# Performance work log

Hardware: AMD Instinct MI355X
Metric: run time of the kernel (lower is better)

The kernel has to match this reference:

```python
import jax, jax.numpy as jnp
import numpy as np

N, D, E = 40000, 128, 640000
SLOPE = 0.01  # torch LeakyReLU default negative_slope

def leaky(x):
    return jnp.where(x >= 0, x, SLOPE * x)

def setup_inputs() -> dict:
    key = jax.random.key(0)
    ks = jax.random.split(key, 12)
    s = lambda fan_in: 1.0 / np.sqrt(fan_in)
    inp = {
        "x": jax.random.normal(ks[0], (N, D), jnp.float32),
        "pos": jax.random.normal(ks[1], (N, 3), jnp.float32),
        "edge_index": jax.random.randint(ks[2], (2, E), 0, N, jnp.int64),
        # mlp_h: Linear(D,D) -> LeakyReLU -> Linear(D,3) -> Tanh
        "Wh1": jax.random.uniform(ks[3], (D, D), jnp.float32, -s(D), s(D)),
        "bh1": jnp.zeros((D,), jnp.float32),
        "Wh2": jax.random.uniform(ks[4], (D, 3), jnp.float32, -s(D), s(D)),
        "bh2": jnp.zeros((3,), jnp.float32),
        # mlp_f: Linear(D+3, D) -> LeakyReLU
        "Wf1": jax.random.uniform(ks[5], (D + 3, D), jnp.float32, -s(D + 3), s(D + 3)),
        "bf1": jnp.zeros((D,), jnp.float32),
        # mlp_g: Linear(D,D) -> LeakyReLU -> Linear(D,D)
        "Wg1": jax.random.uniform(ks[6], (D, D), jnp.float32, -s(D), s(D)),
        "bg1": jnp.zeros((D,), jnp.float32),
        "Wg2": jax.random.uniform(ks[7], (D, D), jnp.float32, -s(D), s(D)),
        "bg2": jnp.zeros((D,), jnp.float32),
    }
    return inp

def reference(x, pos, edge_index, Wh1, bh1, Wh2, bh2, Wf1, bf1, Wg1, bg1, Wg2, bg2):
    src = edge_index[0]  # j (source / neighbor)
    dst = edge_index[1]  # i (target / center)
    n = x.shape[0]
    # mlp_h per node: predicted position offset delta_i
    delta = jnp.tanh(leaky(x @ Wh1 + bh1) @ Wh2 + bh2)  # [N, 3]
    # per-edge message: mlp_f(cat(pos_j - pos_i + delta_i, x_j))
    rel = pos[src] - pos[dst] + delta[dst]               # [E, 3]
    e = jnp.concatenate([rel, x[src]], axis=-1)          # [E, D+3]
    msg = leaky(e @ Wf1 + bf1)                           # [E, D]
    # sum aggregation to target nodes
    aggr = jax.ops.segment_sum(msg, dst, num_segments=n) # [N, D]
    # node update with residual
    out = x + (leaky(aggr @ Wg1 + bg1) @ Wg2 + bg2)      # [N, D]
    return out
```

## Files before the change

### kernel.cpp

```cpp
#include <hip/hip_runtime.h>

#define NN 40000
#define DD 128
#define EE 640000
#define SLOPE 0.01f
#define CAP 64

typedef __attribute__((ext_vector_type(8))) short  short8;
typedef __attribute__((ext_vector_type(8))) unsigned short ushort8;
typedef __attribute__((ext_vector_type(4))) float  floatx4;

__device__ __forceinline__ float leaky1(float v) { return v >= 0.f ? v : v * SLOPE; }

__device__ __forceinline__ unsigned short f2bf(float f) {
    unsigned int u = __float_as_uint(f);
    u += 0x7fffu + ((u >> 16) & 1u);
    return (unsigned short)(u >> 16);
}

__global__ __launch_bounds__(256) void k_init(
    const float* __restrict__ Wh1, const float* __restrict__ Wf1,
    const float* __restrict__ Wg1, const float* __restrict__ Wg2,
    int* __restrict__ cnt, unsigned short* __restrict__ pk)
{
    const int gid = blockIdx.x * 256 + threadIdx.x;
    if (gid < NN) cnt[gid] = 0;

    if (gid < 8192) {
        const int mat = gid >> 11;
        const int rem = gid & 2047;
        const int ct  = rem >> 8;
        const int kc  = (rem >> 6) & 3;
        const int l   = rem & 63;
        const float* W = (mat == 0) ? Wh1 : (mat == 1) ? (Wf1 + 3 * DD)
                       : (mat == 2) ? Wg1 : Wg2;
        const int n  = ct * 16 + (l & 15);
        const int k0 = kc * 32 + (l >> 4) * 8;
        ushort8 v;
        #pragma unroll
        for (int j = 0; j < 8; ++j) v[j] = f2bf(W[(size_t)(k0 + j) * DD + n]);
        *(ushort8*)(pk + (size_t)gid * 8) = v;
    }
}

__global__ __launch_bounds__(512) void k_pre_scatter(
    const float* __restrict__ x,
    const unsigned short* __restrict__ pk,
    const float* __restrict__ pos, const float* __restrict__ Wf1,
    const float* __restrict__ bh1, const float* __restrict__ Wh2,
    const float* __restrict__ bh2, const float* __restrict__ bf1,
    const int* __restrict__ ei,
    unsigned short* __restrict__ ub, float* __restrict__ delta,
    int* __restrict__ cnt, unsigned short* __restrict__ esrc)
{
    __shared__ unsigned short xt[64 * 136];
    __shared__ unsigned short ul[64 * 136];
    const int bid = blockIdx.x;
    const int t   = threadIdx.x;

    if (bid >= 625) {
        const int g   = bid & 7;
        const int lb  = (bid - 625) >> 3;
        const int dlo = g * 5000;
        const int dhi = dlo + 5000;

        for (int e = (lb * 512 + t) * 2; e < EE; e += 262144) {
            const int2 dp = *(const int2*)(ei + EE + e);
            const int2 sp = *(const int2*)(ei + e);
            if (dp.x >= dlo && dp.x < dhi) {
                const int p = atomicAdd(&cnt[dp.x], 1);
                if (p < CAP) esrc[(size_t)dp.x * CAP + p] = (unsigned short)sp.x;
            }
            if (dp.y >= dlo && dp.y < dhi) {
                const int p = atomicAdd(&cnt[dp.y], 1);
                if (p < CAP) esrc[(size_t)dp.y * CAP + p] = (unsigned short)sp.y;
            }
        }
        return;
    }

    const int w  = t >> 6, l = t & 63;
    const int lm = l & 15, q = l >> 4;
    const int rowb = bid * 64;

    {
        const int row = t >> 3;
        const int c0  = (t & 7) * 16;
        const float* xp = x + (size_t)(rowb + row) * DD + c0;
        #pragma unroll
        for (int p = 0; p < 2; ++p) {
            const float4 v0 = *(const float4*)(xp + p * 8);
            const float4 v1 = *(const float4*)(xp + p * 8 + 4);
            ushort8 o;
            o[0] = f2bf(v0.x); o[1] = f2bf(v0.y); o[2] = f2bf(v0.z); o[3] = f2bf(v0.w);
            o[4] = f2bf(v1.x); o[5] = f2bf(v1.y); o[6] = f2bf(v1.z); o[7] = f2bf(v1.w);
            *(ushort8*)(xt + row * 136 + c0 + p * 8) = o;
        }
    }
    __syncthreads();

    const bool upath = w < 4;
    const int wl   = upath ? w : w - 4;
    const int row0 = wl * 16;
    const unsigned short* pkm = upath ? (pk + 16384) : pk;

    floatx4 acc[8];
    #pragma unroll
    for (int ct = 0; ct < 8; ++ct) acc[ct] = 0.f;

    #pragma unroll
    for (int kc = 0; kc < 4; ++kc) {
        const short8 a = *(const short8*)(xt + (row0 + lm) * 136 + kc * 32 + q * 8);
        #pragma unroll
        for (int ct = 0; ct < 8; ++ct) {
            const short8 b = *(const short8*)(pkm + (size_t)((ct * 4 + kc) * 64 + l) * 8);
            acc[ct] = __builtin_amdgcn_mfma_f32_16x16x32_bf16(a, b, acc[ct], 0, 0, 0);
        }
    }

    if (upath) {
        float px[4][3];
        #pragma unroll
        for (int r = 0; r < 4; ++r) {
            const int rr = rowb + row0 + q * 4 + r;
            px[r][0] = pos[rr * 3 + 0];
            px[r][1] = pos[rr * 3 + 1];
            px[r][2] = pos[rr * 3 + 2];
        }
        #pragma unroll
        for (int ct = 0; ct < 8; ++ct) {
            const int col = ct * 16 + lm;
            const float bfv = bf1[col];
            const float w0 = Wf1[0 * DD + col];
            const float w1 = Wf1[1 * DD + col];
            const float w2 = Wf1[2 * DD + col];
            #pragma unroll
            for (int r = 0; r < 4; ++r) {
                const float uv = acc[ct][r] + bfv
                               + px[r][0] * w0 + px[r][1] * w1 + px[r][2] * w2;
                ul[(row0 + q * 4 + r) * 136 + col] = f2bf(uv);
            }
        }
    } else {
        float p[4][3] = {};
        #pragma unroll
        for (int ct = 0; ct < 8; ++ct) {
            const int col = ct * 16 + lm;
            const float b1 = bh1[col];
            const float wh20 = Wh2[col * 3 + 0];
            const float wh21 = Wh2[col * 3 + 1];
            const float wh22 = Wh2[col * 3 + 2];
            #pragma unroll
            for (int r = 0; r < 4; ++r) {
                const float hv = leaky1(acc[ct][r] + b1);
                p[r][0] += hv * wh20;
                p[r][1] += hv * wh21;
                p[r][2] += hv * wh22;
            }
        }
        #pragma unroll
        for (int m = 1; m < 16; m <<= 1) {
            #pragma unroll
            for (int r = 0; r < 4; ++r) {
                #pragma unroll
                for (int k = 0; k < 3; ++k)
                    p[r][k] += __shfl_xor(p[r][k], m);
            }
        }
        if (lm < 12) {
            const int r = lm / 3, k = lm - 3 * (lm / 3);
            delta[(size_t)(rowb + row0 + q * 4 + r) * 3 + k] = tanhf(p[r][k] + bh2[k]);
        }
    }
    __syncthreads();

    #pragma unroll
    for (int k = 0; k < 2; ++k) {
        const int idx = t + k * 512;
        const int row = idx >> 4;
        const int c8  = (idx & 15) * 8;
        *(ushort8*)(ub + (size_t)(rowb + row) * DD + c8) =
            *(const ushort8*)(ul + row * 136 + c8);
    }
}

__global__ __launch_bounds__(256) void k_gather(
    const int* __restrict__ cnt, const unsigned short* __restrict__ esrc,
    const float* __restrict__ pos, const float* __restrict__ delta,
    const float* __restrict__ Wf1, const unsigned short* __restrict__ ub,
    unsigned short* __restrict__ aggrb)
{
    const int t    = threadIdx.x;
    const int lane = t & 63;
    const int n    = blockIdx.x * 4 + (t >> 6);
    const int grp  = lane >> 4;
    const int li   = lane & 15;
    const int c    = li * 8;

    const float q0 = delta[n * 3 + 0] - pos[n * 3 + 0];
    const float q1 = delta[n * 3 + 1] - pos[n * 3 + 1];
    const float q2 = delta[n * 3 + 2] - pos[n * 3 + 2];

    float v[8];
    #pragma unroll
    for (int h = 0; h < 2; ++h) {
        const float4 w0 = *(const float4*)(Wf1 + 0 * DD + c + h * 4);
        const float4 w1 = *(const float4*)(Wf1 + 1 * DD + c + h * 4);
        const float4 w2 = *(const float4*)(Wf1 + 2 * DD + c + h * 4);
        v[h * 4 + 0] = q0 * w0.x + q1 * w1.x + q2 * w2.x;
        v[h * 4 + 1] = q0 * w0.y + q1 * w1.y + q2 * w2.y;
        v[h * 4 + 2] = q0 * w0.z + q1 * w1.z + q2 * w2.z;
        v[h * 4 + 3] = q0 * w0.w + q1 * w1.w + q2 * w2.w;
    }

    const int s_all = (int)esrc[(size_t)n * CAP + lane];
    const int d = min(cnt[n], CAP);

    float a[8] = {0.f, 0.f, 0.f, 0.f, 0.f, 0.f, 0.f, 0.f};

    for (int j = 0; j < d; j += 16) {
        uint4 u[4];
        bool vld[4];
        #pragma unroll
        for (int k = 0; k < 4; ++k) {
            const int e = j + 4 * k + grp;
            vld[k] = e < d;
            int src = __shfl(s_all, e & 63);
            src = vld[k] ? src : 0;
            u[k] = *(const uint4*)(ub + (size_t)src * DD + c);
        }
        #pragma unroll
        for (int k = 0; k < 4; ++k) {
            if (vld[k]) {
                const unsigned int uu0 = u[k].x, uu1 = u[k].y, uu2 = u[k].z, uu3 = u[k].w;
                const float e0 = __uint_as_float(uu0 << 16)         + v[0];
                const float e1 = __uint_as_float(uu0 & 0xffff0000u) + v[1];
                const float e2 = __uint_as_float(uu1 << 16)         + v[2];
                const float e3 = __uint_as_float(uu1 & 0xffff0000u) + v[3];
                const float e4 = __uint_as_float(uu2 << 16)         + v[4];
                const float e5 = __uint_as_float(uu2 & 0xffff0000u) + v[5];
                const float e6 = __uint_as_float(uu3 << 16)         + v[6];
                const float e7 = __uint_as_float(uu3 & 0xffff0000u) + v[7];
                a[0] += fmaxf(e0, e0 * SLOPE);
                a[1] += fmaxf(e1, e1 * SLOPE);
                a[2] += fmaxf(e2, e2 * SLOPE);
                a[3] += fmaxf(e3, e3 * SLOPE);
                a[4] += fmaxf(e4, e4 * SLOPE);
                a[5] += fmaxf(e5, e5 * SLOPE);
                a[6] += fmaxf(e6, e6 * SLOPE);
                a[7] += fmaxf(e7, e7 * SLOPE);
            }
        }
    }

    #pragma unroll
    for (int i = 0; i < 8; ++i) {
        a[i] += __shfl_xor(a[i], 16);
        a[i] += __shfl_xor(a[i], 32);
    }

    if (grp == 0) {
        uint4 st;
        st.x = ((unsigned int)f2bf(a[1]) << 16) | (unsigned int)f2bf(a[0]);
        st.y = ((unsigned int)f2bf(a[3]) << 16) | (unsigned int)f2bf(a[2]);
        st.z = ((unsigned int)f2bf(a[5]) << 16) | (unsigned int)f2bf(a[4]);
        st.w = ((unsigned int)f2bf(a[7]) << 16) | (unsigned int)f2bf(a[6]);
        *(uint4*)(aggrb + (size_t)n * DD + c) = st;
    }
}

__global__ __launch_bounds__(256) void k_node_out(
    const unsigned short* __restrict__ aggrb, const unsigned short* __restrict__ pk,
    const float* __restrict__ x,
    const float* __restrict__ bg1, const float* __restrict__ bg2,
    float* __restrict__ out)
{
    __shared__ unsigned short gl[64 * 136];
    __shared__ float          ol[64 * 132];
    const int t  = threadIdx.x;
    const int w  = t >> 6, l = t & 63;
    const int lm = l & 15, q = l >> 4;
    const int rowb = blockIdx.x * 64;
    const int row0 = rowb + w * 16;

    const unsigned short* pkg1 = pk + 32768;
    const unsigned short* pkg2 = pk + 49152;

    floatx4 gacc[8];
    #pragma unroll
    for (int ct = 0; ct < 8; ++ct) gacc[ct] = 0.f;

    #pragma unroll
    for (int kc = 0; kc < 4; ++kc) {
        const short8 a = *(const short8*)(aggrb + (size_t)(row0 + lm) * DD + kc * 32 + q * 8);
        #pragma unroll
        for (int ct = 0; ct < 8; ++ct) {
            const short8 b = *(const short8*)(pkg1 + (size_t)((ct * 4 + kc) * 64 + l) * 8);
            gacc[ct] = __builtin_amdgcn_mfma_f32_16x16x32_bf16(a, b, gacc[ct], 0, 0, 0);
        }
    }

    #pragma unroll
    for (int ct = 0; ct < 8; ++ct) {
        const int col = ct * 16 + lm;
        const float b1 = bg1[col];
        #pragma unroll
        for (int r = 0; r < 4; ++r)
            gl[(w * 16 + q * 4 + r) * 136 + col] = f2bf(leaky1(gacc[ct][r] + b1));
    }
    __syncthreads();

    floatx4 oacc[8];
    #pragma unroll
    for (int ct = 0; ct < 8; ++ct) oacc[ct] = 0.f;

    #pragma unroll
    for (int kc = 0; kc < 4; ++kc) {
        const short8 a = *(const short8*)(gl + (size_t)(w * 16 + lm) * 136 + kc * 32 + q * 8);
        #pragma unroll
        for (int ct = 0; ct < 8; ++ct) {
            const short8 b = *(const short8*)(pkg2 + (size_t)((ct * 4 + kc) * 64 + l) * 8);
            oacc[ct] = __builtin_amdgcn_mfma_f32_16x16x32_bf16(a, b, oacc[ct], 0, 0, 0);
        }
    }

    __syncthreads();
    #pragma unroll
    for (int ct = 0; ct < 8; ++ct) {
        const int col = ct * 16 + lm;
        #pragma unroll
        for (int r = 0; r < 4; ++r)
            ol[(w * 16 + q * 4 + r) * 132 + col] = oacc[ct][r];
    }
    __syncthreads();

    #pragma unroll
    for (int k = 0; k < 8; ++k) {
        const int idx = t + k * 256;
        const int row = idx >> 5;
        const int c4  = (idx & 31) * 4;
        const float4 ov = *(const float4*)(ol + row * 132 + c4);
        const float4 bv = *(const float4*)(bg2 + c4);
        const size_t o  = (size_t)(rowb + row) * DD + c4;
        const float4 xv = *(const float4*)(x + o);
        float4 rv;
        rv.x = xv.x + ov.x + bv.x;
        rv.y = xv.y + ov.y + bv.y;
        rv.z = xv.z + ov.z + bv.z;
        rv.w = xv.w + ov.w + bv.w;
        *(float4*)(out + o) = rv;
    }
}

extern "C" void kernel_launch(void* const* d_in, const int* in_sizes, int n_in,
                              void* d_out, int out_size, void* d_ws, size_t ws_size,
                              hipStream_t stream)
{
    const float* x   = (const float*)d_in[0];
    const float* pos = (const float*)d_in[1];
    const int*   ei  = (const int*)d_in[2];
    const float* Wh1 = (const float*)d_in[3];
    const float* bh1 = (const float*)d_in[4];
    const float* Wh2 = (const float*)d_in[5];
    const float* bh2 = (const float*)d_in[6];
    const float* Wf1 = (const float*)d_in[7];
    const float* bf1 = (const float*)d_in[8];
    const float* Wg1 = (const float*)d_in[9];
    const float* bg1 = (const float*)d_in[10];
    const float* Wg2 = (const float*)d_in[11];
    const float* bg2 = (const float*)d_in[12];
    float* out = (float*)d_out;

    unsigned short* ub    = (unsigned short*)d_ws;
    unsigned short* aggrb = ub + (size_t)NN * DD;
    unsigned short* pk    = aggrb + (size_t)NN * DD;
    float* delta = (float*)(pk + 65536);
    int*   cnt   = (int*)(delta + (size_t)NN * 3);
    unsigned short* esrc = (unsigned short*)(cnt + NN);

    k_init<<<160, 256, 0, stream>>>(Wh1, Wf1, Wg1, Wg2, cnt, pk);
    k_pre_scatter<<<2673, 512, 0, stream>>>(x, pk, pos, Wf1, bh1, Wh2, bh2, bf1,
                                            ei, ub, delta, cnt, esrc);
    k_gather<<<NN / 4, 256, 0, stream>>>(cnt, esrc, pos, delta, Wf1, ub, aggrb);
    k_node_out<<<NN / 64, 256, 0, stream>>>(aggrb, pk, x, bg1, bg2, out);
}
```

Baseline: 167.7 us.

## Fuse edge gather-aggregation into node output kernel, keeping aggregates in LDS

Merges the per-node gather/aggregation kernel with the node-update MLP kernel. Each wave now aggregates 16 nodes one after another and writes the bf16 sums into shared memory, reusing the output staging buffer. The MFMA GEMMs then read those sums from LDS instead of a global buffer. This removes one launch and the global round trip for the aggregate, but shrinks the grid from 10000 blocks to 625. That leaves far fewer waves in flight to hide latency in the memory-bound gather.

```diff
diff --git a/kernel.cpp b/kernel.cpp
--- a/kernel.cpp
+++ b/kernel.cpp
@@ -184,107 +184,110 @@
     }
 }
 
-__global__ __launch_bounds__(256) void k_gather(
+__global__ __launch_bounds__(256) void k_gather_out(
     const int* __restrict__ cnt, const unsigned short* __restrict__ esrc,
     const float* __restrict__ pos, const float* __restrict__ delta,
     const float* __restrict__ Wf1, const unsigned short* __restrict__ ub,
-    unsigned short* __restrict__ aggrb)
-{
-    const int t    = threadIdx.x;
-    const int lane = t & 63;
-    const int n    = blockIdx.x * 4 + (t >> 6);
-    const int grp  = lane >> 4;
-    const int li   = lane & 15;
-    const int c    = li * 8;
-
-    const float q0 = delta[n * 3 + 0] - pos[n * 3 + 0];
-    const float q1 = delta[n * 3 + 1] - pos[n * 3 + 1];
-    const float q2 = delta[n * 3 + 2] - pos[n * 3 + 2];
-
-    float v[8];
-    #pragma unroll
-    for (int h = 0; h < 2; ++h) {
-        const float4 w0 = *(const float4*)(Wf1 + 0 * DD + c + h * 4);
-        const float4 w1 = *(const float4*)(Wf1 + 1 * DD + c + h * 4);
-        const float4 w2 = *(const float4*)(Wf1 + 2 * DD + c + h * 4);
-        v[h * 4 + 0] = q0 * w0.x + q1 * w1.x + q2 * w2.x;
-        v[h * 4 + 1] = q0 * w0.y + q1 * w1.y + q2 * w2.y;
-        v[h * 4 + 2] = q0 * w0.z + q1 * w1.z + q2 * w2.z;
-        v[h * 4 + 3] = q0 * w0.w + q1 * w1.w + q2 * w2.w;
-    }
-
-    const int s_all = (int)esrc[(size_t)n * CAP + lane];
-    const int d = min(cnt[n], CAP);
-
-    float a[8] = {0.f, 0.f, 0.f, 0.f, 0.f, 0.f, 0.f, 0.f};
-
-    for (int j = 0; j < d; j += 16) {
-        uint4 u[4];
-        bool vld[4];
-        #pragma unroll
-        for (int k = 0; k < 4; ++k) {
-            const int e = j + 4 * k + grp;
-            vld[k] = e < d;
-            int src = __shfl(s_all, e & 63);
-            src = vld[k] ? src : 0;
-            u[k] = *(const uint4*)(ub + (size_t)src * DD + c);
-        }
-        #pragma unroll
-        for (int k = 0; k < 4; ++k) {
-            if (vld[k]) {
-                const unsigned int uu0 = u[k].x, uu1 = u[k].y, uu2 = u[k].z, uu3 = u[k].w;
-                const float e0 = __uint_as_float(uu0 << 16)         + v[0];
-                const float e1 = __uint_as_float(uu0 & 0xffff0000u) + v[1];
-                const float e2 = __uint_as_float(uu1 << 16)         + v[2];
-                const float e3 = __uint_as_float(uu1 & 0xffff0000u) + v[3];
-                const float e4 = __uint_as_float(uu2 << 16)         + v[4];
-                const float e5 = __uint_as_float(uu2 & 0xffff0000u) + v[5];
-                const float e6 = __uint_as_float(uu3 << 16)         + v[6];
-                const float e7 = __uint_as_float(uu3 & 0xffff0000u) + v[7];
-                a[0] += fmaxf(e0, e0 * SLOPE);
-                a[1] += fmaxf(e1, e1 * SLOPE);
-                a[2] += fmaxf(e2, e2 * SLOPE);
-                a[3] += fmaxf(e3, e3 * SLOPE);
-                a[4] += fmaxf(e4, e4 * SLOPE);
-                a[5] += fmaxf(e5, e5 * SLOPE);
-                a[6] += fmaxf(e6, e6 * SLOPE);
-                a[7] += fmaxf(e7, e7 * SLOPE);
-            }
-        }
-    }
-
-    #pragma unroll
-    for (int i = 0; i < 8; ++i) {
-        a[i] += __shfl_xor(a[i], 16);
-        a[i] += __shfl_xor(a[i], 32);
-    }
-
-    if (grp == 0) {
-        uint4 st;
-        st.x = ((unsigned int)f2bf(a[1]) << 16) | (unsigned int)f2bf(a[0]);
-        st.y = ((unsigned int)f2bf(a[3]) << 16) | (unsigned int)f2bf(a[2]);
-        st.z = ((unsigned int)f2bf(a[5]) << 16) | (unsigned int)f2bf(a[4]);
-        st.w = ((unsigned int)f2bf(a[7]) << 16) | (unsigned int)f2bf(a[6]);
-        *(uint4*)(aggrb + (size_t)n * DD + c) = st;
-    }
-}
-
-__global__ __launch_bounds__(256) void k_node_out(
-    const unsigned short* __restrict__ aggrb, const unsigned short* __restrict__ pk,
+    const unsigned short* __restrict__ pk,
     const float* __restrict__ x,
     const float* __restrict__ bg1, const float* __restrict__ bg2,
     float* __restrict__ out)
 {
     __shared__ unsigned short gl[64 * 136];
     __shared__ float          ol[64 * 132];
-    const int t  = threadIdx.x;
-    const int w  = t >> 6, l = t & 63;
-    const int lm = l & 15, q = l >> 4;
+    unsigned short* agg = (unsigned short*)ol;
+
+    const int t    = threadIdx.x;
+    const int w    = t >> 6, l = t & 63;
+    const int lane = l;
+    const int grp  = lane >> 4;
+    const int li   = lane & 15;
+    const int c    = li * 8;
+    const int lm   = l & 15, q = l >> 4;
     const int rowb = blockIdx.x * 64;
-    const int row0 = rowb + w * 16;
+
+    float wf[3][8];
+    #pragma unroll
+    for (int r = 0; r < 3; ++r) {
+        const float4 va = *(const float4*)(Wf1 + r * DD + c);
+        const float4 vb = *(const float4*)(Wf1 + r * DD + c + 4);
+        wf[r][0] = va.x; wf[r][1] = va.y; wf[r][2] = va.z; wf[r][3] = va.w;
+        wf[r][4] = vb.x; wf[r][5] = vb.y; wf[r][6] = vb.z; wf[r][7] = vb.w;
+    }
+
+    for (int nn = 0; nn < 16; ++nn) {
+        const int lrow = w * 16 + nn;
+        const int n    = rowb + lrow;
+
+        const float q0 = delta[n * 3 + 0] - pos[n * 3 + 0];
+        const float q1 = delta[n * 3 + 1] - pos[n * 3 + 1];
+        const float q2 = delta[n * 3 + 2] - pos[n * 3 + 2];
+
+        float v[8];
+        #pragma unroll
+        for (int i = 0; i < 8; ++i)
+            v[i] = q0 * wf[0][i] + q1 * wf[1][i] + q2 * wf[2][i];
+
+        const int s_all = (int)esrc[(size_t)n * CAP + lane];
+        const int d = min(cnt[n], CAP);
+
+        float a[8] = {0.f, 0.f, 0.f, 0.f, 0.f, 0.f, 0.f, 0.f};
+
+        for (int j = 0; j < d; j += 16) {
+            uint4 u[4];
+            bool vld[4];
+            #pragma unroll
+            for (int k = 0; k < 4; ++k) {
+                const int e = j + 4 * k + grp;
+                vld[k] = e < d;
+                int src = __shfl(s_all, e & 63);
+                src = vld[k] ? src : 0;
+                u[k] = *(const uint4*)(ub + (size_t)src * DD + c);
+            }
+            #pragma unroll
+            for (int k = 0; k < 4; ++k) {
+                if (vld[k]) {
+                    const unsigned int uu0 = u[k].x, uu1 = u[k].y, uu2 = u[k].z, uu3 = u[k].w;
+                    const float e0 = __uint_as_float(uu0 << 16)         + v[0];
+                    const float e1 = __uint_as_float(uu0 & 0xffff0000u) + v[1];
+                    const float e2 = __uint_as_float(uu1 << 16)         + v[2];
+                    const float e3 = __uint_as_float(uu1 & 0xffff0000u) + v[3];
+                    const float e4 = __uint_as_float(uu2 << 16)         + v[4];
+                    const float e5 = __uint_as_float(uu2 & 0xffff0000u) + v[5];
+                    const float e6 = __uint_as_float(uu3 << 16)         + v[6];
+                    const float e7 = __uint_as_float(uu3 & 0xffff0000u) + v[7];
+                    a[0] += fmaxf(e0, e0 * SLOPE);
+                    a[1] += fmaxf(e1, e1 * SLOPE);
+                    a[2] += fmaxf(e2, e2 * SLOPE);
+                    a[3] += fmaxf(e3, e3 * SLOPE);
+                    a[4] += fmaxf(e4, e4 * SLOPE);
+                    a[5] += fmaxf(e5, e5 * SLOPE);
+                    a[6] += fmaxf(e6, e6 * SLOPE);
+                    a[7] += fmaxf(e7, e7 * SLOPE);
+                }
+            }
+        }
+
+        #pragma unroll
+        for (int i = 0; i < 8; ++i) {
+            a[i] += __shfl_xor(a[i], 16);
+            a[i] += __shfl_xor(a[i], 32);
+        }
+
+        if (grp == 0) {
+            uint4 st;
+            st.x = ((unsigned int)f2bf(a[1]) << 16) | (unsigned int)f2bf(a[0]);
+            st.y = ((unsigned int)f2bf(a[3]) << 16) | (unsigned int)f2bf(a[2]);
+            st.z = ((unsigned int)f2bf(a[5]) << 16) | (unsigned int)f2bf(a[4]);
+            st.w = ((unsigned int)f2bf(a[7]) << 16) | (unsigned int)f2bf(a[6]);
+            *(uint4*)(agg + (size_t)lrow * 136 + c) = st;
+        }
+    }
+    __syncthreads();
 
     const unsigned short* pkg1 = pk + 32768;
     const unsigned short* pkg2 = pk + 49152;
+    const int lr0 = w * 16;
 
     floatx4 gacc[8];
     #pragma unroll
@@ -292,7 +295,7 @@
 
     #pragma unroll
     for (int kc = 0; kc < 4; ++kc) {
-        const short8 a = *(const short8*)(aggrb + (size_t)(row0 + lm) * DD + kc * 32 + q * 8);
+        const short8 a = *(const short8*)(agg + (size_t)(lr0 + lm) * 136 + kc * 32 + q * 8);
         #pragma unroll
         for (int ct = 0; ct < 8; ++ct) {
             const short8 b = *(const short8*)(pkg1 + (size_t)((ct * 4 + kc) * 64 + l) * 8);
@@ -371,9 +374,8 @@
     const float* bg2 = (const float*)d_in[12];
     float* out = (float*)d_out;
 
-    unsigned short* ub    = (unsigned short*)d_ws;
-    unsigned short* aggrb = ub + (size_t)NN * DD;
-    unsigned short* pk    = aggrb + (size_t)NN * DD;
+    unsigned short* ub   = (unsigned short*)d_ws;
+    unsigned short* pk   = ub + (size_t)NN * DD;
     float* delta = (float*)(pk + 65536);
     int*   cnt   = (int*)(delta + (size_t)NN * 3);
     unsigned short* esrc = (unsigned short*)(cnt + NN);
@@ -381,6 +383,6 @@
     k_init<<<160, 256, 0, stream>>>(Wh1, Wf1, Wg1, Wg2, cnt, pk);
     k_pre_scatter<<<2673, 512, 0, stream>>>(x, pk, pos, Wf1, bh1, Wh2, bh2, bf1,
                                             ei, ub, delta, cnt, esrc);
-    k_gather<<<NN / 4, 256, 0, stream>>>(cnt, esrc, pos, delta, Wf1, ub, aggrb);
-    k_node_out<<<NN / 64, 256, 0, stream>>>(aggrb, pk, x, bg1, bg2, out);
-}
+    k_gather_out<<<625, 256, 0, stream>>>(cnt, esrc, pos, delta, Wf1, ub, pk,
+                                          x, bg1, bg2, out);
+}
```

Result: slower. 182.3 us (+8.7%).
